# Kernel optimization log

Hardware: AMD Instinct MI355X
Metric: run time of the kernel (lower is better)

The kernel has to match this reference:

```python
import jax, jax.numpy as jnp
import numpy as np

VOCAB, D_IN, D_H = 32000, 512, 1024
B, T = 16, 256
PAD_IDX = 0


def setup_inputs() -> dict:
    key = jax.random.key(0)
    k1, k2, k3, k4, k5 = jax.random.split(key, 5)
    input_idx = jax.random.randint(k1, (B, T), 0, VOCAB, dtype=jnp.int64)
    emb = jax.random.normal(k2, (VOCAB, D_IN), dtype=jnp.float32) * 0.02
    emb = emb.at[PAD_IDX].set(0.0)  # padding_idx row is zero
    weight_x = jax.random.normal(k3, (D_H, D_IN), dtype=jnp.float32) * (1.0 / np.sqrt(D_IN))
    weight_h = jax.random.normal(k4, (D_H, D_H), dtype=jnp.float32) * (1.0 / np.sqrt(D_H))
    bias = jnp.zeros((D_H,), dtype=jnp.float32)
    lm_W = jax.random.normal(k5, (VOCAB, D_H), dtype=jnp.float32) * (1.0 / np.sqrt(D_H))
    return {"input_idx": input_idx, "emb": emb, "weight_x": weight_x,
            "weight_h": weight_h, "bias": bias, "lm_W": lm_W}


def reference(input_idx, emb, weight_x, weight_h, bias, lm_W):
    Bsz = input_idx.shape[0]
    h0 = jnp.zeros((Bsz, weight_h.shape[0]), dtype=weight_x.dtype)

    def step(h, tok):
        x = emb[tok]  # [B, D_IN]
        h_new = jnp.tanh(x @ weight_x.T + h @ weight_h.T + bias)
        mask = (tok != PAD_IDX)[:, None]  # keep old h at pad positions
        h = jnp.where(mask, h_new, h)
        return h, h

    _, h_all = jax.lax.scan(step, h0, input_idx.T)  # [T, B, H]
    h_all = jnp.swapaxes(h_all, 0, 1)               # [B, T, H]
    logits = jnp.einsum('bth,vh->btv', h_all, lm_W)  # [B, T, V]
    return logits
```

## Files before the change

kernel.cpp:

```cpp
#include <hip/hip_runtime.h>

#define PAD_IDX 0

typedef __attribute__((ext_vector_type(8))) short short8;
typedef __attribute__((ext_vector_type(4))) float f32x4;

__device__ __forceinline__ unsigned short f32_to_bf16_rne(float f) {
  unsigned int u = __builtin_bit_cast(unsigned int, f);
  u += 0x7FFFu + ((u >> 16) & 1u);
  return (unsigned short)(u >> 16);
}

__device__ __forceinline__ void load16_to_lds(const void* g, void* lds) {
  __builtin_amdgcn_global_load_lds(
      (const __attribute__((address_space(1))) unsigned int*)g,
      (__attribute__((address_space(3))) unsigned int*)lds,
      16, 0, 0);
}

__global__ void sentinel_kernel(float* out) { out[0] = 1.0e6f; }

__global__ __launch_bounds__(256) void xwcvt_kernel(const int* __restrict__ tok,
                                                    const float* __restrict__ emb,
                                                    const float* __restrict__ Wx,
                                                    const float* __restrict__ bias,
                                                    float* __restrict__ xw,
                                                    const float* __restrict__ lmW,
                                                    unsigned short* __restrict__ lmW_bf) {
  int tid = threadIdx.x;
  if (blockIdx.x >= 1024) {
    const int n8 = 32000 * 1024 / 8;
    int stride = 512 * 256;
    for (int i = (blockIdx.x - 1024) * 256 + tid; i < n8; i += stride) {
      float4 a = ((const float4*)lmW)[2 * i];
      float4 b = ((const float4*)lmW)[2 * i + 1];
      ushort4 lo, hi;
      lo.x = f32_to_bf16_rne(a.x); lo.y = f32_to_bf16_rne(a.y);
      lo.z = f32_to_bf16_rne(a.z); lo.w = f32_to_bf16_rne(a.w);
      hi.x = f32_to_bf16_rne(b.x); hi.y = f32_to_bf16_rne(b.y);
      hi.z = f32_to_bf16_rne(b.z); hi.w = f32_to_bf16_rne(b.w);
      ((ushort4*)lmW_bf)[2 * i] = lo;
      ((ushort4*)lmW_bf)[2 * i + 1] = hi;
    }
    return;
  }
  __shared__ float At[32][68];
  __shared__ float Bt[32][68];
  __shared__ int stok[64];
  int tm = blockIdx.x & 63;
  int tn = blockIdx.x >> 6;
  int r0 = tm * 64, j0 = tn * 64;
  if (tid < 64) stok[tid] = tok[r0 + tid];
  int tx = tid & 15, ty = tid >> 4;
  float acc[4][4] = {};
  for (int kt = 0; kt < 512; kt += 32) {
    __syncthreads();
    #pragma unroll
    for (int ii = 0; ii < 2; ++ii) {
      int idx = tid * 2 + ii;
      int m = idx >> 3, fv = idx & 7;
      float4 va = *(const float4*)&emb[(size_t)stok[m] * 512 + kt + fv * 4];
      float4 vb = *(const float4*)&Wx[(size_t)(j0 + m) * 512 + kt + fv * 4];
      At[fv * 4 + 0][m] = va.x; At[fv * 4 + 1][m] = va.y;
      At[fv * 4 + 2][m] = va.z; At[fv * 4 + 3][m] = va.w;
      Bt[fv * 4 + 0][m] = vb.x; Bt[fv * 4 + 1][m] = vb.y;
      Bt[fv * 4 + 2][m] = vb.z; Bt[fv * 4 + 3][m] = vb.w;
    }
    __syncthreads();
    #pragma unroll
    for (int k = 0; k < 32; ++k) {
      float4 a4 = *(const float4*)&At[k][ty * 4];
      float4 b4 = *(const float4*)&Bt[k][tx * 4];
      float av[4] = {a4.x, a4.y, a4.z, a4.w};
      float bv[4] = {b4.x, b4.y, b4.z, b4.w};
      #pragma unroll
      for (int i = 0; i < 4; ++i)
        #pragma unroll
        for (int jj = 0; jj < 4; ++jj) acc[i][jj] = fmaf(av[i], bv[jj], acc[i][jj]);
    }
  }
  #pragma unroll
  for (int i = 0; i < 4; ++i) {
    size_t row = (size_t)(r0 + ty * 4 + i) * 1024 + j0 + tx * 4;
    #pragma unroll
    for (int jj = 0; jj < 4; ++jj)
      xw[row + jj] = acc[i][jj] + bias[j0 + tx * 4 + jj];
  }
}

__global__ __launch_bounds__(1024, 4) void rec_kernel(const float* __restrict__ Wh,
                                                      const float* __restrict__ xw,
                                                      const int* __restrict__ tok,
                                                      unsigned long long* hcomb,
                                                      unsigned short* __restrict__ h_all) {
  int c = blockIdx.x & 15;
  int g = blockIdx.x >> 4;
  int tid = threadIdx.x;
  int w = tid >> 6;
  int l = tid & 63;
  int j = g * 64 + l;

  const float* wb = Wh + (size_t)j * 1024 + w * 64;
#define LDW(i) f32x4 w##i = *(const f32x4*)(wb + i * 4);
  LDW(0) LDW(1) LDW(2) LDW(3) LDW(4) LDW(5) LDW(6) LDW(7)
  LDW(8) LDW(9) LDW(10) LDW(11) LDW(12) LDW(13) LDW(14) LDW(15)
#undef LDW

  __shared__ float hs[16][64];
  __shared__ float pbuf[16][64];
  unsigned long long* hc0 = hcomb + (size_t)c * 1024;
  unsigned long long* hc1 = hcomb + 16 * 1024 + (size_t)c * 1024;
  bool writer = (w == 0);
  float prevh = 0.f;

  for (int t = 0; t < 256; ++t) {
    float xv = 0.f;
    int tkn = 1;
    if (writer) {
      xv = xw[((size_t)c * 256 + t) * 1024 + j];
      tkn = tok[c * 256 + t];
    }
    unsigned long long* src = ((t & 1) ? hc1 : hc0) + tid;
    unsigned long long v;
    int guard = 0;
    do {
      v = __hip_atomic_load(src, __ATOMIC_RELAXED, __HIP_MEMORY_SCOPE_AGENT);
      if ((unsigned int)(v >> 32) == (unsigned int)t) break;
      __builtin_amdgcn_s_sleep(1);
    } while (++guard < (1 << 20));
    hs[w][l] = __builtin_bit_cast(float, (unsigned int)v);
    __asm__ volatile("s_waitcnt lgkmcnt(0)" ::: "memory");

    const float* hp = &hs[w][0];
    f32x4 a0 = {0.f, 0.f, 0.f, 0.f}, a1 = a0, a2 = a0, a3 = a0;
#define FMAI(i, acc) { f32x4 h4 = *(const f32x4*)(hp + i * 4); acc += w##i * h4; }
    FMAI(0, a0) FMAI(1, a1) FMAI(2, a2) FMAI(3, a3)
    FMAI(4, a0) FMAI(5, a1) FMAI(6, a2) FMAI(7, a3)
    FMAI(8, a0) FMAI(9, a1) FMAI(10, a2) FMAI(11, a3)
    FMAI(12, a0) FMAI(13, a1) FMAI(14, a2) FMAI(15, a3)
#undef FMAI
    f32x4 aa = (a0 + a1) + (a2 + a3);
    pbuf[w][l] = (aa[0] + aa[1]) + (aa[2] + aa[3]);
    __asm__ volatile("s_waitcnt lgkmcnt(0)\n\ts_barrier" ::: "memory");

    if (writer) {
      float s = 0.f;
      #pragma unroll
      for (int q = 0; q < 16; ++q) s += pbuf[q][l];
      float hnew;
      if (tkn != PAD_IDX) {
        float pre = xv + s;
        float e = __builtin_amdgcn_exp2f(pre * 2.8853900817779268f);
        hnew = 1.0f - 2.0f / (e + 1.0f);
      } else {
        hnew = prevh;
      }
      prevh = hnew;
      unsigned long long pv =
          ((unsigned long long)(unsigned int)(t + 1) << 32) |
          (unsigned long long)__builtin_bit_cast(unsigned int, hnew);
      __hip_atomic_store((((t + 1) & 1) ? hc1 : hc0) + j, pv,
                         __ATOMIC_RELAXED, __HIP_MEMORY_SCOPE_AGENT);
      h_all[((size_t)c * 256 + t) * 1024 + j] = f32_to_bf16_rne(hnew);
    }
  }
}

__global__ __launch_bounds__(512) void gemm_kernel(const unsigned short* __restrict__ A,
                                                   const unsigned short* __restrict__ B,
                                                   float* __restrict__ C) {
  __shared__ unsigned short lds[2 * 32768];
  int tid = threadIdx.x;
  int lane = tid & 63, wave = tid >> 6;
  int bid = blockIdx.x;
  int x = bid & 7;
  int r = bid >> 3;
  int tm = 2 * x + (r & 1);
  int tn = r >> 1;
  int r0 = tm * 256, c0 = tn * 256;
  int wm = wave >> 2, wn = wave & 3;

  auto STAGE = [&](int kt, int st) {
    unsigned short* bufA = (unsigned short*)lds + st * 32768;
    unsigned short* bufB = bufA + 16384;
    #pragma unroll
    for (int i = 0; i < 4; ++i) {
      int slot = i * 512 + tid;
      int row = slot >> 3, sg = slot & 7;
      int kg = sg ^ (row & 7);
      const unsigned short* ga = A + (size_t)(r0 + row) * 1024 + kt * 64 + kg * 8;
      load16_to_lds(ga, &bufA[(i * 512 + wave * 64) * 8]);
    }
    #pragma unroll
    for (int i = 0; i < 4; ++i) {
      int slot = i * 512 + tid;
      int row = slot >> 3, sg = slot & 7;
      int kg = sg ^ (row & 7);
      const unsigned short* gb = B + (size_t)(c0 + row) * 1024 + kt * 64 + kg * 8;
      load16_to_lds(gb, &bufB[(i * 512 + wave * 64) * 8]);
    }
  };

  f32x4 zero = {0.f, 0.f, 0.f, 0.f};
  f32x4 acc[8][4];
  #pragma unroll
  for (int i = 0; i < 8; ++i)
    #pragma unroll
    for (int jx = 0; jx < 4; ++jx) acc[i][jx] = zero;

  STAGE(0, 0);
  STAGE(1, 1);
  __asm__ volatile("s_waitcnt vmcnt(8)\n\ts_barrier" ::: "memory");

  for (int kt = 0; kt < 16; ++kt) {
    int st = kt & 1;
    const unsigned short* bufA = (const unsigned short*)lds + st * 32768;
    const unsigned short* bufB = bufA + 16384;

    short8 af[8][2], bf[4][2];
    #pragma unroll
    for (int kkb = 0; kkb < 2; ++kkb) {
      int kbyte = kkb * 64 + (lane >> 4) * 16;
      #pragma unroll
      for (int i = 0; i < 8; ++i) {
        int rowa = wm * 128 + i * 16 + (lane & 15);
        af[i][kkb] = *(const short8*)((const char*)bufA + rowa * 128 + (kbyte ^ ((rowa & 7) << 4)));
      }
      #pragma unroll
      for (int i = 0; i < 4; ++i) {
        int rowb = wn * 64 + i * 16 + (lane & 15);
        bf[i][kkb] = *(const short8*)((const char*)bufB + rowb * 128 + (kbyte ^ ((rowb & 7) << 4)));
      }
    }
    __asm__ volatile("s_waitcnt lgkmcnt(0)\n\ts_barrier" ::: "memory");
    if (kt < 14) {
      STAGE(kt + 2, st);
    } else {
      unsigned short* dead = (unsigned short*)lds + st * 32768;
      #pragma unroll
      for (int i = 0; i < 8; ++i) load16_to_lds(A + (size_t)r0 * 1024, &dead[i * 8]);
    }
    __builtin_amdgcn_s_setprio(1);
    #pragma unroll
    for (int kkb = 0; kkb < 2; ++kkb)
      #pragma unroll
      for (int i = 0; i < 8; ++i)
        #pragma unroll
        for (int jx = 0; jx < 4; ++jx)
          acc[i][jx] = __builtin_amdgcn_mfma_f32_16x16x32_bf16(af[i][kkb], bf[jx][kkb], acc[i][jx], 0, 0, 0);
    __builtin_amdgcn_s_setprio(0);
    __asm__ volatile("s_waitcnt vmcnt(8)\n\ts_barrier" ::: "memory");
  }
  __asm__ volatile("s_waitcnt vmcnt(0)" ::: "memory");

  int rbase = r0 + wm * 128 + (lane >> 4) * 4;
  int cbase = c0 + wn * 64 + (lane & 15);
  #pragma unroll
  for (int i = 0; i < 8; ++i)
    #pragma unroll
    for (int jx = 0; jx < 4; ++jx)
      #pragma unroll
      for (int q = 0; q < 4; ++q)
        C[(size_t)(rbase + i * 16 + q) * 32000 + cbase + jx * 16] = acc[i][jx][q];
}

extern "C" void kernel_launch(void* const* d_in, const int* in_sizes, int n_in,
                              void* d_out, int out_size, void* d_ws, size_t ws_size,
                              hipStream_t stream) {
  const int* tok = (const int*)d_in[0];
  const float* emb = (const float*)d_in[1];
  const float* Wx = (const float*)d_in[2];
  const float* Wh = (const float*)d_in[3];
  const float* bias = (const float*)d_in[4];
  const float* lmW = (const float*)d_in[5];
  float* out = (float*)d_out;

  const size_t OFF_LMW = 0;
  const size_t OFF_XW = 65536000;
  const size_t OFF_HALL = OFF_XW + 16777216;
  const size_t OFF_HCMB = OFF_HALL + 8388608;
  const size_t NEED = OFF_HCMB + 262144;
  if (ws_size < NEED) {
    sentinel_kernel<<<1, 1, 0, stream>>>(out);
    return;
  }
  char* ws = (char*)d_ws;
  unsigned short* lmW_bf = (unsigned short*)(ws + OFF_LMW);
  float* xw = (float*)(ws + OFF_XW);
  unsigned short* h_all = (unsigned short*)(ws + OFF_HALL);
  unsigned long long* hcomb = (unsigned long long*)(ws + OFF_HCMB);

  hipMemsetAsync(ws + OFF_HCMB, 0, 262144, stream);
  xwcvt_kernel<<<1536, 256, 0, stream>>>(tok, emb, Wx, bias, xw, lmW, lmW_bf);
  rec_kernel<<<256, 1024, 0, stream>>>(Wh, xw, tok, hcomb, h_all);
  gemm_kernel<<<2000, 512, 0, stream>>>(h_all, lmW_bf, out);
}
```

Measured before the change: 869.3 us.

## Split GEMM main loop into four phases interleaving half-tile loads with MFMA

Restructures the LM-head GEMM K-loop into four sub-phases (k-half by B-column-half). Each phase interleaves LDS fragment reads, a half-tile global-to-LDS prefetch and a smaller MFMA cluster, with the B and A prefetch stages offset by one iteration. This follows a ping-pong style schedule meant to overlap memory traffic with matrix math and cut register pressure from holding whole fragments. The cost is many more barriers per iteration, and the tricky buffer reuse ordering could cause races or stalls.

```diff
diff --git a/kernel.cpp b/kernel.cpp
--- a/kernel.cpp
+++ b/kernel.cpp
@@ -180,24 +180,17 @@
   int r0 = tm * 256, c0 = tn * 256;
   int wm = wave >> 2, wn = wave & 3;
 
-  auto STAGE = [&](int kt, int st) {
-    unsigned short* bufA = (unsigned short*)lds + st * 32768;
-    unsigned short* bufB = bufA + 16384;
-    #pragma unroll
-    for (int i = 0; i < 4; ++i) {
+  auto SH = [&](int kt, int st, int mat, int half) {
+    unsigned short* buf = (unsigned short*)lds + st * 32768 + mat * 16384 + half * 8192;
+    const unsigned short* src = mat ? (B + (size_t)(c0 + half * 128) * 1024)
+                                    : (A + (size_t)(r0 + half * 128) * 1024);
+    #pragma unroll
+    for (int i = 0; i < 2; ++i) {
       int slot = i * 512 + tid;
       int row = slot >> 3, sg = slot & 7;
       int kg = sg ^ (row & 7);
-      const unsigned short* ga = A + (size_t)(r0 + row) * 1024 + kt * 64 + kg * 8;
-      load16_to_lds(ga, &bufA[(i * 512 + wave * 64) * 8]);
-    }
-    #pragma unroll
-    for (int i = 0; i < 4; ++i) {
-      int slot = i * 512 + tid;
-      int row = slot >> 3, sg = slot & 7;
-      int kg = sg ^ (row & 7);
-      const unsigned short* gb = B + (size_t)(c0 + row) * 1024 + kt * 64 + kg * 8;
-      load16_to_lds(gb, &bufB[(i * 512 + wave * 64) * 8]);
+      const unsigned short* g = src + (size_t)row * 1024 + kt * 64 + kg * 8;
+      load16_to_lds(g, &buf[(i * 512 + wave * 64) * 8]);
     }
   };
 
@@ -208,48 +201,99 @@
     #pragma unroll
     for (int jx = 0; jx < 4; ++jx) acc[i][jx] = zero;
 
-  STAGE(0, 0);
-  STAGE(1, 1);
-  __asm__ volatile("s_waitcnt vmcnt(8)\n\ts_barrier" ::: "memory");
+  SH(0, 0, 0, 0); SH(0, 0, 0, 1); SH(0, 0, 1, 0); SH(0, 0, 1, 1);
+  SH(1, 1, 0, 0); SH(1, 1, 0, 1);
+  __asm__ volatile("s_waitcnt vmcnt(0)" ::: "memory");
+  __builtin_amdgcn_s_barrier();
 
   for (int kt = 0; kt < 16; ++kt) {
     int st = kt & 1;
-    const unsigned short* bufA = (const unsigned short*)lds + st * 32768;
-    const unsigned short* bufB = bufA + 16384;
-
-    short8 af[8][2], bf[4][2];
-    #pragma unroll
-    for (int kkb = 0; kkb < 2; ++kkb) {
-      int kbyte = kkb * 64 + (lane >> 4) * 16;
-      #pragma unroll
-      for (int i = 0; i < 8; ++i) {
-        int rowa = wm * 128 + i * 16 + (lane & 15);
-        af[i][kkb] = *(const short8*)((const char*)bufA + rowa * 128 + (kbyte ^ ((rowa & 7) << 4)));
-      }
-      #pragma unroll
-      for (int i = 0; i < 4; ++i) {
-        int rowb = wn * 64 + i * 16 + (lane & 15);
-        bf[i][kkb] = *(const short8*)((const char*)bufB + rowb * 128 + (kbyte ^ ((rowb & 7) << 4)));
-      }
-    }
-    __asm__ volatile("s_waitcnt lgkmcnt(0)\n\ts_barrier" ::: "memory");
-    if (kt < 14) {
-      STAGE(kt + 2, st);
-    } else {
-      unsigned short* dead = (unsigned short*)lds + st * 32768;
-      #pragma unroll
-      for (int i = 0; i < 8; ++i) load16_to_lds(A + (size_t)r0 * 1024, &dead[i * 8]);
-    }
+    const char* bufA = (const char*)((const unsigned short*)lds + st * 32768);
+    const char* bufB = bufA + 32768;
+    int ktB = kt + 1 > 15 ? 15 : kt + 1;
+    int ktA = kt + 2 > 15 ? 15 : kt + 2;
+    int kb0 = (lane >> 4) * 16;
+    int kb1 = 64 + kb0;
+    short8 af0[8], af1[8], bf0[4], bf1[4];
+
+    #pragma unroll
+    for (int i = 0; i < 8; ++i) {
+      int rowa = wm * 128 + i * 16 + (lane & 15);
+      af0[i] = *(const short8*)(bufA + rowa * 128 + (kb0 ^ ((rowa & 7) << 4)));
+    }
+    #pragma unroll
+    for (int jx = 0; jx < 2; ++jx) {
+      int rowb = wn * 64 + jx * 16 + (lane & 15);
+      bf0[jx] = *(const short8*)(bufB + rowb * 128 + (kb0 ^ ((rowb & 7) << 4)));
+    }
+    SH(ktB, st ^ 1, 1, 0);
+    __builtin_amdgcn_s_barrier();
+    __asm__ volatile("s_waitcnt lgkmcnt(0)" ::: "memory");
     __builtin_amdgcn_s_setprio(1);
     #pragma unroll
-    for (int kkb = 0; kkb < 2; ++kkb)
-      #pragma unroll
-      for (int i = 0; i < 8; ++i)
-        #pragma unroll
-        for (int jx = 0; jx < 4; ++jx)
-          acc[i][jx] = __builtin_amdgcn_mfma_f32_16x16x32_bf16(af[i][kkb], bf[jx][kkb], acc[i][jx], 0, 0, 0);
+    for (int i = 0; i < 8; ++i)
+      #pragma unroll
+      for (int jx = 0; jx < 2; ++jx)
+        acc[i][jx] = __builtin_amdgcn_mfma_f32_16x16x32_bf16(af0[i], bf0[jx], acc[i][jx], 0, 0, 0);
     __builtin_amdgcn_s_setprio(0);
-    __asm__ volatile("s_waitcnt vmcnt(8)\n\ts_barrier" ::: "memory");
+    __builtin_amdgcn_s_barrier();
+
+    #pragma unroll
+    for (int jx = 2; jx < 4; ++jx) {
+      int rowb = wn * 64 + jx * 16 + (lane & 15);
+      bf0[jx] = *(const short8*)(bufB + rowb * 128 + (kb0 ^ ((rowb & 7) << 4)));
+    }
+    SH(ktB, st ^ 1, 1, 1);
+    __builtin_amdgcn_s_barrier();
+    __asm__ volatile("s_waitcnt lgkmcnt(0)" ::: "memory");
+    __builtin_amdgcn_s_setprio(1);
+    #pragma unroll
+    for (int i = 0; i < 8; ++i)
+      #pragma unroll
+      for (int jx = 2; jx < 4; ++jx)
+        acc[i][jx] = __builtin_amdgcn_mfma_f32_16x16x32_bf16(af0[i], bf0[jx], acc[i][jx], 0, 0, 0);
+    __builtin_amdgcn_s_setprio(0);
+    __builtin_amdgcn_s_barrier();
+
+    #pragma unroll
+    for (int i = 0; i < 8; ++i) {
+      int rowa = wm * 128 + i * 16 + (lane & 15);
+      af1[i] = *(const short8*)(bufA + rowa * 128 + (kb1 ^ ((rowa & 7) << 4)));
+    }
+    #pragma unroll
+    for (int jx = 0; jx < 2; ++jx) {
+      int rowb = wn * 64 + jx * 16 + (lane & 15);
+      bf1[jx] = *(const short8*)(bufB + rowb * 128 + (kb1 ^ ((rowb & 7) << 4)));
+    }
+    __builtin_amdgcn_s_barrier();
+    __asm__ volatile("s_waitcnt lgkmcnt(0)" ::: "memory");
+    __builtin_amdgcn_s_setprio(1);
+    #pragma unroll
+    for (int i = 0; i < 8; ++i)
+      #pragma unroll
+      for (int jx = 0; jx < 2; ++jx)
+        acc[i][jx] = __builtin_amdgcn_mfma_f32_16x16x32_bf16(af1[i], bf1[jx], acc[i][jx], 0, 0, 0);
+    __builtin_amdgcn_s_setprio(0);
+    __builtin_amdgcn_s_barrier();
+
+    #pragma unroll
+    for (int jx = 2; jx < 4; ++jx) {
+      int rowb = wn * 64 + jx * 16 + (lane & 15);
+      bf1[jx] = *(const short8*)(bufB + rowb * 128 + (kb1 ^ ((rowb & 7) << 4)));
+    }
+    SH(ktA, st, 0, 0);
+    SH(ktA, st, 0, 1);
+    __builtin_amdgcn_s_barrier();
+    __asm__ volatile("s_waitcnt lgkmcnt(0)" ::: "memory");
+    __builtin_amdgcn_s_setprio(1);
+    #pragma unroll
+    for (int i = 0; i < 8; ++i)
+      #pragma unroll
+      for (int jx = 2; jx < 4; ++jx)
+        acc[i][jx] = __builtin_amdgcn_mfma_f32_16x16x32_bf16(af1[i], bf1[jx], acc[i][jx], 0, 0, 0);
+    __builtin_amdgcn_s_setprio(0);
+    __asm__ volatile("s_waitcnt vmcnt(4)" ::: "memory");
+    __builtin_amdgcn_s_barrier();
   }
   __asm__ volatile("s_waitcnt vmcnt(0)" ::: "memory");
 
```

New measurement: 868.4 us. No clear change (-0.1%).
